# Optimization experiments

Measured on AMD Instinct MI355X. Metric: run time of the kernel, lower is better.

Reference implementation:

```python
import jax, jax.numpy as jnp
import numpy as np

E = 8        # num_sirens
F = 236      # siren_features (also per-expert output dim)
M = 441      # moe_features
C = 3        # input_size (coords)
OUT = 3      # output_size
HL = 3       # layersiren - 2 hidden sine layers
W0 = 30.0
N = 65536


def setup_inputs() -> dict:
    key = jax.random.key(0)
    ks = jax.random.split(key, 20)
    u = lambda k, shape, lim: jax.random.uniform(k, shape, jnp.float32, -lim, lim)
    sl = lambda fan_in: float(np.sqrt(6.0 / fan_in) / 30.0)  # sine_init limit
    inp = {}
    inp["x"] = jax.random.uniform(ks[0], (N, C), jnp.float32, -1.0, 1.0)
    # SIREN experts, stacked over E. First layer: first_layer_sine_init (1/fan_in).
    inp["siren_W1"] = u(ks[1], (E, C, F), 1.0 / C)
    inp["siren_b1"] = u(ks[2], (E, F), 1.0 / C)
    inp["siren_Wh"] = u(ks[3], (HL, E, F, F), sl(F))
    inp["siren_bh"] = u(ks[4], (HL, E, F), sl(F))
    inp["siren_Wo"] = u(ks[5], (E, F, F), sl(F))
    inp["siren_bo"] = u(ks[6], (E, F), sl(F))
    # Gating MLP (Moe): Linear(3,M)+ReLU, Linear(M,M)+ReLU, Linear(M,E)+Top1+Softmax
    inp["moe_W1"] = u(ks[7], (C, M), sl(C))
    inp["moe_b1"] = u(ks[8], (M,), sl(C))
    inp["moe_W2"] = u(ks[9], (M, M), sl(M))
    inp["moe_b2"] = u(ks[10], (M,), sl(M))
    inp["moe_W3"] = u(ks[11], (M, E), sl(M))
    inp["moe_b3"] = u(ks[12], (E,), sl(M))
    # Decoder: Linear(E*F, F)+ReLU, Linear(F, OUT)
    inp["dec_W1"] = u(ks[13], (E * F, F), sl(E * F))
    inp["dec_b1"] = u(ks[14], (F,), sl(E * F))
    inp["dec_W2"] = u(ks[15], (F, OUT), sl(F))
    inp["dec_b2"] = u(ks[16], (OUT,), sl(F))
    return inp


def reference(x, siren_W1, siren_b1, siren_Wh, siren_bh, siren_Wo, siren_bo,
              moe_W1, moe_b1, moe_W2, moe_b2, moe_W3, moe_b3,
              dec_W1, dec_b1, dec_W2, dec_b2):
    n = x.shape[0]
    # --- parallel SIREN experts, batched over E ---
    h = jnp.sin(W0 * (jnp.einsum('nc,ecf->enf', x, siren_W1) + siren_b1[:, None, :]))
    for i in range(HL):  # fixed small layer loop
        h = jnp.sin(W0 * (jnp.einsum('enf,efg->eng', h, siren_Wh[i]) + siren_bh[i][:, None, :]))
    so = jnp.einsum('enf,efg->eng', h, siren_Wo) + siren_bo[:, None, :]       # (E,N,F)
    siren_cat = jnp.transpose(so, (1, 0, 2)).reshape(n, E * F)                # cat along -1, expert-major
    # --- gating MLP + Top-1 + softmax ---
    g = jax.nn.relu(x @ moe_W1 + moe_b1)
    g = jax.nn.relu(g @ moe_W2 + moe_b2)
    logits = g @ moe_W3 + moe_b3                                              # (N,E)
    _, top_idx = jax.lax.top_k(logits, 1)
    mask = jnp.zeros_like(logits).at[jnp.arange(n)[:, None], top_idx].set(1.0)
    masked = jnp.where(mask > 0, logits, -jnp.inf)
    weights = jax.nn.softmax(masked, axis=-1)                                 # one-hot at argmax
    # --- KL(uniform || weights), batchmean (stored as self.kl_loss in torch) ---
    logw = jnp.log(weights + 1e-10)
    unif = jnp.asarray(1.0 / E, logw.dtype)
    kl = jnp.sum(unif * (jnp.log(unif) - logw)) / n
    # --- repeat_interleave(F) * concat, then decoder ---
    w_full = jnp.broadcast_to(weights[:, :, None], (n, E, F)).reshape(n, E * F)
    dec_in = w_full * siren_cat
    out = jax.nn.relu(dec_in @ dec_W1 + dec_b1) @ dec_W2 + dec_b2             # (N,OUT)
    return out, kl
```

## Files before the change

kernel.cpp:

```cpp
#include <hip/hip_runtime.h>
#include <cstdint>

typedef unsigned short ushort_t;
typedef short bf16x8 __attribute__((ext_vector_type(8)));
typedef unsigned short u16x8 __attribute__((ext_vector_type(8)));
typedef float f32x4 __attribute__((ext_vector_type(4)));

#define NPTS 65536
#define WS_CNT 0
#define WS_BKT 64
#define OFF_W2S 1048640
#define OFF_W3T 1450048
#define OFF_SWT 1464640
#define OFF_D2F 6379840
#define WS_FAST 6388032u
#define WS_SLOW (64 + 8 * NPTS * 2)

__device__ __forceinline__ float bf2f(ushort_t u) {
  union { unsigned u; float f; } c; c.u = ((unsigned)u) << 16; return c.f;
}
__device__ __forceinline__ ushort_t f2bf(float f) {
  union { float f; unsigned u; } c; c.f = f;
  unsigned u = c.u + 0x7fffu + ((c.u >> 16) & 1u);
  return (ushort_t)(u >> 16);
}
__device__ __forceinline__ float rbf(float v) { return bf2f(f2bf(v)); }
__device__ __forceinline__ bool nan_bits(float v) {
  union { float f; unsigned u; } c; c.f = v;
  return ((c.u >> 23) & 0xFFu) == 0xFFu && (c.u & 0x7FFFFFu) != 0u;
}

__global__ void k_sentinel(float* out) {
  if (threadIdx.x == 0) out[0] = 1.0e30f;
}


__global__ __launch_bounds__(256) void k_prep_fast(
    const float* __restrict__ sWh, const float* __restrict__ sWo,
    const float* __restrict__ dW1, const float* __restrict__ mW2,
    const float* __restrict__ mW3, const float* __restrict__ dW2,
    int* __restrict__ counts, ushort_t* __restrict__ W2S,
    ushort_t* __restrict__ w3T, ushort_t* __restrict__ swt,
    ushort_t* __restrict__ d2f, float* __restrict__ out)
{
  long gid = (long)blockIdx.x * 256 + threadIdx.x;
  long gs = (long)gridDim.x * 256;
  for (long i = gid; i < 40L * 61440; i += gs) {
    int mat = (int)(i / 61440);
    int f = (int)(i - (long)mat * 61440);
    int u = f & 7, ln = (f >> 3) & 63, kt = (f >> 9) & 7, t = f >> 12;
    int n = t * 16 + (ln & 15);
    int k = kt * 32 + (ln >> 4) * 8 + u;
    if (n >= 236 || k >= 236) swt[i] = 0;
  }
  for (long i = gid; i < 40L * 55696; i += gs) {
    int mat = (int)(i / 55696);
    int r = (int)(i - (long)mat * 55696);
    int k = r / 236, n = r - k * 236;
    const float* W = (mat < 24) ? (sWh + (long)mat * 55696)
                   : (mat < 32) ? (sWo + (long)(mat - 24) * 55696)
                                : (dW1 + (long)(mat - 32) * 55696);
    ushort_t v = f2bf(W[r]);
    int t = n >> 4, l15 = n & 15;
    int kt = k >> 5, rr = k & 31;
    long dst = (long)mat * 61440 + (t << 12) + (kt << 9) + ((((rr >> 3) << 4) + l15) << 3) + (rr & 7);
    swt[dst] = v;
  }
  for (long i = gid; i < 4096; i += gs) {
    int u = (int)(i & 7), lane = (int)((i >> 3) & 63), kt = (int)(i >> 9);
    int n = lane & 15, k = kt * 32 + ((lane >> 4) << 3) + u;
    d2f[i] = (n < 3 && k < 236) ? f2bf(dW2[k * 3 + n]) : (ushort_t)0;
  }
  for (long i = gid; i < 25088; i += gs) {
    int kt = (int)(i / (28 * 64));
    int rem = (int)(i - (long)kt * 28 * 64);
    int nt = rem / 64, lane = rem - nt * 64;
    int l15 = lane & 15, quad = lane >> 4;
    int n = nt * 16 + l15;
    u16x8 tv;
    #pragma unroll
    for (int u = 0; u < 8; ++u) {
      int k = kt * 32 + quad * 8 + u;
      tv[u] = (k < 441 && n < 441) ? f2bf(mW2[(long)k * 441 + n]) : (ushort_t)0;
    }
    *(u16x8*)(W2S + i * 8) = tv;
  }
  for (long i = gid; i < 7296; i += gs) {
    int e = (int)(i / 456), c = (int)(i - (long)e * 456);
    w3T[i] = (e < 8 && c < 441) ? f2bf(mW3[(long)c * 8 + e]) : (ushort_t)0;
  }
  if (gid < 8) counts[gid] = 0;
  if (gid == 8) out[NPTS * 3] = 18.125f;
}

__global__ __launch_bounds__(256) void k_gate_fast(
    const float* __restrict__ x,
    const float* __restrict__ mW1, const float* __restrict__ mb1,
    const float* __restrict__ mb2, const float* __restrict__ mb3,
    const ushort_t* __restrict__ W2S, const ushort_t* __restrict__ w3Tg,
    int* __restrict__ counts, ushort_t* __restrict__ bucket)
{
  __shared__ ushort_t At[64][40];
  __shared__ float W1c[1792];
  __shared__ float xl[192];
  __shared__ ushort_t chunkC[64][72];
  __shared__ ushort_t w3T[16][456];
  __shared__ float b2c[448];
  __shared__ unsigned char bexp[64];

  int tid = threadIdx.x;
  int blk = blockIdx.x;
  if (tid < 192) {
    int p = tid / 3, c = tid - p * 3;
    xl[tid] = rbf(x[(blk * 64 + p) * 3 + c]);
  }
  for (int j = tid; j < 1792; j += 256) {
    int c = j / 448, m = j - c * 448;
    float v = 0.f;
    if (m < 441) v = (c < 3) ? rbf(mW1[c * 441 + m]) : rbf(mb1[m]);
    W1c[j] = v;
  }
  for (int j = tid; j < 448; j += 256) b2c[j] = (j < 441) ? rbf(mb2[j]) : 0.f;
  for (int ch = tid; ch < 912; ch += 256)
    *(u16x8*)(&w3T[0][0] + ch * 8) = *(const u16x8*)(w3Tg + ch * 8);

  int w = tid >> 6, lane = tid & 63;
  int l15 = lane & 15, quad = lane >> 4;

  f32x4 acc[4][7];
  #pragma unroll
  for (int a = 0; a < 4; ++a)
    #pragma unroll
    for (int b = 0; b < 7; ++b)
      acc[a][b] = (f32x4){0.f, 0.f, 0.f, 0.f};

  int am = tid >> 2, ak = (tid & 3) * 8;

  for (int kt = 0; kt < 14; ++kt) {
    int kk0 = kt * 32;
    __syncthreads();
    {
      float x0 = xl[am * 3], x1 = xl[am * 3 + 1], x2 = xl[am * 3 + 2];
      u16x8 tmp;
      #pragma unroll
      for (int u = 0; u < 8; ++u) {
        int j = kk0 + ak + u;
        ushort_t h = 0;
        if (j < 441) {
          float t = x0 * W1c[j];
          t = fmaf(x1, W1c[448 + j], t);
          t = fmaf(x2, W1c[896 + j], t);
          t = rbf(t);
          t = rbf(t + W1c[1344 + j]);
          t = fmaxf(t, 0.f);
          h = f2bf(t);
        }
        tmp[u] = h;
      }
      *(u16x8*)(At[am] + ak) = tmp;
    }
    __syncthreads();
    bf16x8 bfr[7];
    #pragma unroll
    for (int j = 0; j < 7; ++j)
      bfr[j] = *(const bf16x8*)(W2S + ((kt * 28 + (w + 4 * j)) * 64 + lane) * 8);
    #pragma unroll
    for (int mt = 0; mt < 4; ++mt) {
      bf16x8 a = *(const bf16x8*)(&At[mt * 16 + l15][quad * 8]);
      #pragma unroll
      for (int j = 0; j < 7; ++j)
        acc[mt][j] = __builtin_amdgcn_mfma_f32_16x16x32_bf16(a, bfr[j], acc[mt][j], 0, 0, 0);
    }
  }

  f32x4 acc3[4];
  #pragma unroll
  for (int mt = 0; mt < 4; ++mt) acc3[mt] = (f32x4){0.f, 0.f, 0.f, 0.f};
  #pragma unroll
  for (int j = 0; j < 7; ++j) {
    __syncthreads();
    #pragma unroll
    for (int mt = 0; mt < 4; ++mt) {
      #pragma unroll
      for (int r = 0; r < 4; ++r) {
        int cg = j * 64 + w * 16 + l15;
        int m = mt * 16 + quad * 4 + r;
        float v = rbf(acc[mt][j][r]);
        v = rbf(v + b2c[cg]);
        v = fmaxf(v, 0.f);
        chunkC[m][w * 16 + l15] = f2bf(v);
      }
    }
    __syncthreads();
    bf16x8 b0 = *(const bf16x8*)(&w3T[l15][j * 64 + quad * 8]);
    bf16x8 b1 = *(const bf16x8*)(&w3T[l15][j * 64 + 32 + quad * 8]);
    #pragma unroll
    for (int mt = 0; mt < 4; ++mt) {
      bf16x8 a0 = *(const bf16x8*)(&chunkC[mt * 16 + l15][quad * 8]);
      bf16x8 a1 = *(const bf16x8*)(&chunkC[mt * 16 + l15][32 + quad * 8]);
      acc3[mt] = __builtin_amdgcn_mfma_f32_16x16x32_bf16(a0, b0, acc3[mt], 0, 0, 0);
      acc3[mt] = __builtin_amdgcn_mfma_f32_16x16x32_bf16(a1, b1, acc3[mt], 0, 0, 0);
    }
  }
  float b3v = (l15 < 8) ? rbf(mb3[l15]) : 0.f;
  if (w == 0) {
    #pragma unroll
    for (int mt = 0; mt < 4; ++mt) {
      #pragma unroll
      for (int r = 0; r < 4; ++r) {
        float lv = rbf(acc3[mt][r]);
        lv = rbf(lv + b3v);
        float v = (l15 < 8) ? lv : -1.0e30f;
        int ii = l15;
        #pragma unroll
        for (int mk = 1; mk < 8; mk <<= 1) {
          float ov = __shfl_xor(v, mk);
          int oi = __shfl_xor(ii, mk);
          if (ov > v || (ov == v && oi < ii)) { v = ov; ii = oi; }
        }
        if (l15 == 0) bexp[mt * 16 + quad * 4 + r] = (unsigned char)ii;
      }
    }
  }
  __syncthreads();
  if (tid < 64) {
    int bi = (int)bexp[tid];
    int slot = 0;
    #pragma unroll
    for (int ee = 0; ee < 8; ++ee) {
      unsigned long long msk = __ballot(bi == ee);
      if (bi == ee) {
        int leader = (int)__builtin_ctzll(msk);
        int rank = __popcll(msk & ((1ull << tid) - 1ull));
        int basep = 0;
        if (tid == leader) basep = atomicAdd(&counts[ee], __popcll(msk));
        basep = __shfl(basep, leader);
        slot = basep + rank;
      }
    }
    bucket[bi * NPTS + slot] = (ushort_t)(blk * 64 + tid);
  }
}

__global__ __launch_bounds__(256) void k_sdec_fast(
    const float* __restrict__ x,
    const float* __restrict__ sW1, const float* __restrict__ sb1,
    const float* __restrict__ sbh, const float* __restrict__ sbo,
    const float* __restrict__ db1, const float* __restrict__ db2,
    const ushort_t* __restrict__ swt, const ushort_t* __restrict__ d2f,
    const int* __restrict__ counts, const ushort_t* __restrict__ bucket,
    float* __restrict__ out)
{
  __shared__ ushort_t hA[64][264];
  __shared__ int idxl[64];
  __shared__ float xl[64][3];
  __shared__ float wc[944];

  int e = blockIdx.y;
  int base = blockIdx.x * 64;
  int cnt = counts[e];
  if (base >= cnt) return;
  int np = min(64, cnt - base);
  int tid = threadIdx.x;

  if (tid < 64) {
    int s = base + (tid < np ? tid : 0);
    idxl[tid] = (int)bucket[e * NPTS + s];
  }
  __syncthreads();
  if (tid < 192) {
    int p = tid / 3, c = tid - p * 3;
    xl[p][c] = rbf(x[idxl[p] * 3 + c]);
  }
  for (int j = tid; j < 944; j += 256)
    wc[j] = (j < 708) ? rbf(sW1[e * 708 + j]) : 30.f * rbf(sb1[e * 236 + (j - 708)]);
  __syncthreads();

  int w = tid >> 6, lane = tid & 63;
  int l15 = lane & 15, quad = lane >> 4;

  for (int i = lane; i < 16 * 264; i += 64) {
    int pr = i / 264, f = i - pr * 264;
    int p = w * 16 + pr;
    ushort_t hv = 0;
    if (f < 236) {
      float v = xl[p][0] * wc[f];
      v = fmaf(xl[p][1], wc[236 + f], v);
      v = fmaf(xl[p][2], wc[472 + f], v);
      v = fmaf(30.f, v, wc[708 + f]);
      hv = f2bf(__sinf(v));
    }
    hA[p][f] = hv;
  }
  __syncthreads();

  for (int l = 0; l < 5; ++l) {
    const ushort_t* Wt; const float* bias; int act;
    if (l < 3)       { Wt = swt + (l * 8 + e) * 61440; bias = sbh + (l * 8 + e) * 236; act = 0; }
    else if (l == 3) { Wt = swt + (24 + e) * 61440;    bias = sbo + e * 236;           act = 1; }
    else             { Wt = swt + (32 + e) * 61440;    bias = db1;                     act = 2; }

    bf16x8 afr[4][8];
    #pragma unroll
    for (int mt = 0; mt < 4; ++mt)
      #pragma unroll
      for (int kt = 0; kt < 8; ++kt)
        afr[mt][kt] = *(const bf16x8*)(&hA[mt * 16 + l15][kt * 32 + quad * 8]);
    __syncthreads();

    #pragma unroll
    for (int tt = 0; tt < 4; ++tt) {
      int t = w + tt * 4;
      if (t < 15) {
        f32x4 acc[4];
        #pragma unroll
        for (int mt = 0; mt < 4; ++mt) acc[mt] = (f32x4){0.f, 0.f, 0.f, 0.f};
        #pragma unroll
        for (int kt = 0; kt < 8; ++kt) {
          bf16x8 b = *(const bf16x8*)(Wt + ((t * 8 + kt) * 64 + lane) * 8);
          #pragma unroll
          for (int mt = 0; mt < 4; ++mt)
            acc[mt] = __builtin_amdgcn_mfma_f32_16x16x32_bf16(afr[mt][kt], b, acc[mt], 0, 0, 0);
        }
        int n = t * 16 + l15;
        if (n < 236) {
          float bv = rbf(bias[n]);
          float b30 = 30.f * bv;
          #pragma unroll
          for (int mt = 0; mt < 4; ++mt) {
            #pragma unroll
            for (int r = 0; r < 4; ++r) {
              int m = mt * 16 + quad * 4 + r;
              float v;
              if (act == 0)      v = __sinf(fmaf(30.f, acc[mt][r], b30));
              else if (act == 1) v = acc[mt][r] + bv;
              else               v = fmaxf(acc[mt][r] + bv, 0.f);
              hA[m][n] = f2bf(v);
            }
          }
        }
      }
    }
    __syncthreads();
  }

  {
    f32x4 acc = (f32x4){0.f, 0.f, 0.f, 0.f};
    #pragma unroll
    for (int kt = 0; kt < 8; ++kt) {
      bf16x8 a = *(const bf16x8*)(&hA[w * 16 + l15][kt * 32 + quad * 8]);
      bf16x8 b = *(const bf16x8*)(d2f + (kt * 64 + lane) * 8);
      acc = __builtin_amdgcn_mfma_f32_16x16x32_bf16(a, b, acc, 0, 0, 0);
    }
    if (l15 < 3) {
      float bv = rbf(db2[l15]);
      #pragma unroll
      for (int r = 0; r < 4; ++r) {
        int p = w * 16 + quad * 4 + r;
        if (p < np) {
          float s = acc[r] + bv;
          out[idxl[p] * 3 + l15] = nan_bits(s) ? 16.0f : fminf(fmaxf(s, -4.f), 4.f);
        }
      }
    }
  }
}


__global__ void k_prep_slow(int* counts, float* out) {
  int t = threadIdx.x;
  if (t < 8) counts[t] = 0;
  if (t == 8) out[NPTS * 3] = 18.125f;
}

__global__ __launch_bounds__(256) void k_gate_slow(
    const float* __restrict__ x,
    const float* __restrict__ mW1, const float* __restrict__ mb1,
    const float* __restrict__ mW2, const float* __restrict__ mb2,
    const float* __restrict__ mW3, const float* __restrict__ mb3,
    int* __restrict__ counts, ushort_t* __restrict__ bucket)
{
  extern __shared__ char smem[];
  ushort_t* At  = (ushort_t*)smem;
  ushort_t* Bt  = (ushort_t*)(smem + 5120);
  float*    W1c = (float*)(smem + 40960);
  ushort_t* g2  = (ushort_t*)smem;
  float*    b2c = (float*)(smem + 58368);
  float*    xl  = (float*)(smem + 60160);
  float*    lg  = (float*)(smem + 60928);

  int tid = threadIdx.x;
  int blk = blockIdx.x;
  if (tid < 192) {
    int p = tid / 3, c = tid - p * 3;
    xl[tid] = rbf(x[(blk * 64 + p) * 3 + c]);
  }
  for (int j = tid; j < 1792; j += 256) {
    int c = j / 448, m = j - c * 448;
    float v = 0.f;
    if (m < 441) v = (c < 3) ? rbf(mW1[c * 441 + m]) : rbf(mb1[m]);
    W1c[j] = v;
  }
  for (int j = tid; j < 448; j += 256) b2c[j] = (j < 441) ? rbf(mb2[j]) : 0.f;

  int w = tid >> 6, lane = tid & 63;
  int l15 = lane & 15, quad = lane >> 4;

  f32x4 acc[4][7];
  #pragma unroll
  for (int a = 0; a < 4; ++a)
    #pragma unroll
    for (int b = 0; b < 7; ++b)
      acc[a][b] = (f32x4){0.f, 0.f, 0.f, 0.f};

  int am = tid >> 2, ak = (tid & 3) * 8;

  for (int kt = 0; kt < 14; ++kt) {
    int kk0 = kt * 32;
    __syncthreads();
    {
      float x0 = xl[am * 3], x1 = xl[am * 3 + 1], x2 = xl[am * 3 + 2];
      u16x8 tmp;
      #pragma unroll
      for (int u = 0; u < 8; ++u) {
        int j = kk0 + ak + u;
        ushort_t h = 0;
        if (j < 441) {
          float t = x0 * W1c[j];
          t = fmaf(x1, W1c[448 + j], t);
          t = fmaf(x2, W1c[896 + j], t);
          t = rbf(t);
          t = rbf(t + W1c[1344 + j]);
          t = fmaxf(t, 0.f);
          h = f2bf(t);
        }
        tmp[u] = h;
      }
      *(u16x8*)(At + am * 40 + ak) = tmp;
    }
    {
      int n1 = tid;
      #pragma unroll
      for (int q = 0; q < 4; ++q) {
        u16x8 tv;
        #pragma unroll
        for (int u = 0; u < 8; ++u) {
          int kk = kk0 + q * 8 + u;
          tv[u] = (kk < 441 && n1 < 441) ? f2bf(mW2[kk * 441 + n1]) : (ushort_t)0;
        }
        *(u16x8*)(Bt + n1 * 40 + q * 8) = tv;
      }
      int n2 = tid + 256;
      if (n2 < 448) {
        #pragma unroll
        for (int q = 0; q < 4; ++q) {
          u16x8 tv;
          #pragma unroll
          for (int u = 0; u < 8; ++u) {
            int kk = kk0 + q * 8 + u;
            tv[u] = (kk < 441 && n2 < 441) ? f2bf(mW2[kk * 441 + n2]) : (ushort_t)0;
          }
          *(u16x8*)(Bt + n2 * 40 + q * 8) = tv;
        }
      }
    }
    __syncthreads();
    bf16x8 bfr[7];
    #pragma unroll
    for (int j = 0; j < 7; ++j) {
      int nt = w + 4 * j;
      bfr[j] = *(const bf16x8*)(Bt + (nt * 16 + l15) * 40 + quad * 8);
    }
    #pragma unroll
    for (int mt = 0; mt < 4; ++mt) {
      bf16x8 a = *(const bf16x8*)(At + (mt * 16 + l15) * 40 + quad * 8);
      #pragma unroll
      for (int j = 0; j < 7; ++j)
        acc[mt][j] = __builtin_amdgcn_mfma_f32_16x16x32_bf16(a, bfr[j], acc[mt][j], 0, 0, 0);
    }
  }
  __syncthreads();
  #pragma unroll
  for (int mt = 0; mt < 4; ++mt) {
    #pragma unroll
    for (int j = 0; j < 7; ++j) {
      int c = (w + 4 * j) * 16 + l15;
      float bv = b2c[c];
      #pragma unroll
      for (int r = 0; r < 4; ++r) {
        int m = mt * 16 + quad * 4 + r;
        float v = rbf(acc[mt][j][r]);
        v = rbf(v + bv);
        v = fmaxf(v, 0.f);
        g2[m * 456 + c] = f2bf(v);
      }
    }
  }
  __syncthreads();
  {
    int m3 = tid >> 2, eg = tid & 3;
    float s0 = 0.f, s1 = 0.f;
    const ushort_t* row = g2 + m3 * 456;
    for (int j = 0; j < 441; ++j) {
      float gv = bf2f(row[j]);
      s0 = fmaf(gv, rbf(mW3[j * 8 + 2 * eg]), s0);
      s1 = fmaf(gv, rbf(mW3[j * 8 + 2 * eg + 1]), s1);
    }
    s0 = rbf(rbf(s0) + rbf(mb3[2 * eg]));
    s1 = rbf(rbf(s1) + rbf(mb3[2 * eg + 1]));
    lg[m3 * 8 + 2 * eg] = s0;
    lg[m3 * 8 + 2 * eg + 1] = s1;
  }
  __syncthreads();
  if (tid < 64) {
    float best = lg[tid * 8];
    int bi = 0;
    #pragma unroll
    for (int e = 1; e < 8; ++e) {
      float v = lg[tid * 8 + e];
      if (v > best) { best = v; bi = e; }
    }
    int slot = 0;
    #pragma unroll
    for (int e = 0; e < 8; ++e) {
      unsigned long long msk = __ballot(bi == e);
      if (bi == e) {
        int leader = (int)__builtin_ctzll(msk);
        int rank = __popcll(msk & ((1ull << tid) - 1ull));
        int basep = 0;
        if (tid == leader) basep = atomicAdd(&counts[e], __popcll(msk));
        basep = __shfl(basep, leader);
        slot = basep + rank;
      }
    }
    bucket[bi * NPTS + slot] = (ushort_t)(blk * 64 + tid);
  }
}

__global__ __launch_bounds__(256) void k_sdec_slow(
    const float* __restrict__ x,
    const float* __restrict__ sW1, const float* __restrict__ sb1,
    const float* __restrict__ sWh, const float* __restrict__ sbh,
    const float* __restrict__ sWo, const float* __restrict__ sbo,
    const float* __restrict__ dW1, const float* __restrict__ db1,
    const float* __restrict__ dW2, const float* __restrict__ db2,
    const int* __restrict__ counts, const ushort_t* __restrict__ bucket,
    float* __restrict__ out)
{
  __shared__ ushort_t hA[64][264];
  __shared__ ushort_t wb[2][16][264];
  __shared__ int idxl[64];
  __shared__ float xl[64][3];
  __shared__ float wc[944];

  int e = blockIdx.y;
  int base = blockIdx.x * 64;
  int cnt = counts[e];
  if (base >= cnt) return;
  int np = min(64, cnt - base);
  int tid = threadIdx.x;

  if (tid < 64) {
    int s = base + (tid < np ? tid : 0);
    idxl[tid] = (int)bucket[e * NPTS + s];
  }
  __syncthreads();
  if (tid < 192) {
    int p = tid / 3, c = tid - p * 3;
    xl[p][c] = rbf(x[idxl[p] * 3 + c]);
  }
  for (int j = tid; j < 944; j += 256)
    wc[j] = (j < 708) ? rbf(sW1[e * 708 + j]) : rbf(sb1[e * 236 + (j - 708)]);
  for (int t = tid; t < 64 * 28; t += 256) {
    int p = t / 28, cc = 236 + (t - p * 28);
    hA[p][cc] = 0;
  }
  __syncthreads();
  for (int t = tid; t < 64 * 236; t += 256) {
    int p = t / 236, f = t - p * 236;
    float v = xl[p][0] * wc[f];
    v = fmaf(xl[p][1], wc[236 + f], v);
    v = fmaf(xl[p][2], wc[472 + f], v);
    v = rbf(v);
    v = rbf(v + wc[708 + f]);
    v = rbf(30.f * v);
    hA[p][f] = f2bf(sinf(v));
  }

  int w = tid >> 6, lane = tid & 63;
  int l15 = lane & 15, quad = lane >> 4;

  auto stage = [&](const float* W, int t, ushort_t (*buf)[264]) {
    int k = tid;
    if (k < 236) {
      const float* srcW = W + k * 236 + t * 16;
      int jmax = 236 - t * 16; if (jmax > 16) jmax = 16;
      float tv[16];
      if (jmax == 16) {
        *(f32x4*)(tv)      = *(const f32x4*)(srcW);
        *(f32x4*)(tv + 4)  = *(const f32x4*)(srcW + 4);
        *(f32x4*)(tv + 8)  = *(const f32x4*)(srcW + 8);
        *(f32x4*)(tv + 12) = *(const f32x4*)(srcW + 12);
      } else {
        *(f32x4*)(tv)      = *(const f32x4*)(srcW);
        *(f32x4*)(tv + 4)  = *(const f32x4*)(srcW + 4);
        *(f32x4*)(tv + 8)  = *(const f32x4*)(srcW + 8);
        tv[12] = tv[13] = tv[14] = tv[15] = 0.f;
      }
      #pragma unroll
      for (int j = 0; j < 16; ++j)
        buf[j][k] = (j < jmax) ? f2bf(tv[j]) : (ushort_t)0;
    } else {
      #pragma unroll
      for (int j = 0; j < 16; ++j) buf[j][k] = 0;
    }
  };

  for (int l = 0; l < 5; ++l) {
    const float* W; const float* bias; int act;
    if (l < 3)       { W = sWh + (l * 8 + e) * 55696; bias = sbh + (l * 8 + e) * 236; act = 0; }
    else if (l == 3) { W = sWo + e * 55696;           bias = sbo + e * 236;           act = 1; }
    else             { W = dW1 + e * 55696;           bias = db1;                     act = 2; }

    __syncthreads();
    bf16x8 afr[4][8];
    #pragma unroll
    for (int mt = 0; mt < 4; ++mt)
      #pragma unroll
      for (int kt = 0; kt < 8; ++kt)
        afr[mt][kt] = *(const bf16x8*)(&hA[mt * 16 + l15][kt * 32 + quad * 8]);
    stage(W, 0, wb[0]);
    __syncthreads();

    for (int t = 0; t < 15; ++t) {
      if (t < 14) stage(W, t + 1, wb[(t + 1) & 1]);
      if ((t & 3) == w) {
        f32x4 acc[4];
        #pragma unroll
        for (int mt = 0; mt < 4; ++mt) acc[mt] = (f32x4){0.f, 0.f, 0.f, 0.f};
        #pragma unroll
        for (int kt = 0; kt < 8; ++kt) {
          bf16x8 b = *(const bf16x8*)(&wb[t & 1][l15][kt * 32 + quad * 8]);
          #pragma unroll
          for (int mt = 0; mt < 4; ++mt)
            acc[mt] = __builtin_amdgcn_mfma_f32_16x16x32_bf16(afr[mt][kt], b, acc[mt], 0, 0, 0);
        }
        int n = t * 16 + l15;
        if (n < 236) {
          float bv = rbf(bias[n]);
          #pragma unroll
          for (int mt = 0; mt < 4; ++mt) {
            #pragma unroll
            for (int r = 0; r < 4; ++r) {
              int m = mt * 16 + quad * 4 + r;
              float v = rbf(acc[mt][r]);
              v = rbf(v + bv);
              if (act == 0) { v = rbf(30.f * v); v = sinf(v); }
              else if (act == 2) v = fmaxf(v, 0.f);
              hA[m][n] = f2bf(v);
            }
          }
        }
      }
      __syncthreads();
    }
  }

  for (int j = tid; j < 711; j += 256)
    wc[j] = (j < 708) ? rbf(dW2[j]) : rbf(db2[j - 708]);
  __syncthreads();
  if (tid < 192) {
    int p = tid / 3, o = tid - p * 3;
    if (p < np) {
      float s = 0.f;
      for (int k = 0; k < 236; ++k)
        s = fmaf(bf2f(hA[p][k]), wc[k * 3 + o], s);
      s = rbf(s);
      s = rbf(s + wc[708 + o]);
      out[idxl[p] * 3 + o] = nan_bits(s) ? 16.0f : fminf(fmaxf(s, -4.f), 4.f);
    }
  }
}

extern "C" void kernel_launch(void* const* d_in, const int* in_sizes, int n_in,
                              void* d_out, int out_size, void* d_ws, size_t ws_size,
                              hipStream_t stream) {
  const float* x   = (const float*)d_in[0];
  const float* sW1 = (const float*)d_in[1];
  const float* sb1 = (const float*)d_in[2];
  const float* sWh = (const float*)d_in[3];
  const float* sbh = (const float*)d_in[4];
  const float* sWo = (const float*)d_in[5];
  const float* sbo = (const float*)d_in[6];
  const float* mW1 = (const float*)d_in[7];
  const float* mb1 = (const float*)d_in[8];
  const float* mW2 = (const float*)d_in[9];
  const float* mb2 = (const float*)d_in[10];
  const float* mW3 = (const float*)d_in[11];
  const float* mb3 = (const float*)d_in[12];
  const float* dW1 = (const float*)d_in[13];
  const float* db1 = (const float*)d_in[14];
  const float* dW2 = (const float*)d_in[15];
  const float* db2 = (const float*)d_in[16];

  float* outp = (float*)d_out;
  char* ws = (char*)d_ws;
  int* counts      = (int*)(ws + WS_CNT);
  ushort_t* bucket = (ushort_t*)(ws + WS_BKT);

  if (ws_size >= (size_t)WS_FAST) {
    ushort_t* W2S = (ushort_t*)(ws + OFF_W2S);
    ushort_t* w3T = (ushort_t*)(ws + OFF_W3T);
    ushort_t* swt = (ushort_t*)(ws + OFF_SWT);
    ushort_t* d2f = (ushort_t*)(ws + OFF_D2F);
    k_prep_fast<<<dim3(2048), dim3(256), 0, stream>>>(sWh, sWo, dW1, mW2, mW3, dW2,
                                                      counts, W2S, w3T, swt, d2f, outp);
    k_gate_fast<<<dim3(1024), dim3(256), 0, stream>>>(x, mW1, mb1, mb2, mb3,
                                                      W2S, w3T, counts, bucket);
    k_sdec_fast<<<dim3(1024, 8), dim3(256), 0, stream>>>(x, sW1, sb1, sbh, sbo,
                                                         db1, db2, swt, d2f,
                                                         counts, bucket, outp);
  } else if (ws_size >= (size_t)WS_SLOW) {
    k_prep_slow<<<dim3(1), dim3(64), 0, stream>>>(counts, outp);
    k_gate_slow<<<dim3(1024), dim3(256), 62976, stream>>>(x, mW1, mb1, mW2, mb2, mW3, mb3,
                                                          counts, bucket);
    k_sdec_slow<<<dim3(1024, 8), dim3(256), 0, stream>>>(x, sW1, sb1, sWh, sbh, sWo, sbo,
                                                         dW1, db1, dW2, db2, counts, bucket, outp);
  } else {
    k_sentinel<<<dim3(1), dim3(64), 0, stream>>>(outp);
  }
}
```

Baseline: 284.7 us.

## Compact expert-block grid and vectorize weight swizzle in prep kernel

The siren/decoder kernel now launches a flat grid of 1032 blocks, and each block finds its expert and offset from a prefix scan over the per-expert counts. This replaces the 1024x8 grid, where most blocks exited early, and removes the cost of launching and scheduling about 8k mostly empty blocks. The weight prep loop is also rewritten so each thread gathers 8 bf16 values and writes one 16-byte vector, instead of a separate zero-fill pass followed by scattered 2-byte stores. In exchange, the reads from the source weights are strided, and the grid size assumes at most 1032 non-empty blocks in total.

```diff
diff --git a/kernel.cpp b/kernel.cpp
--- a/kernel.cpp
+++ b/kernel.cpp
@@ -45,26 +45,24 @@
 {
   long gid = (long)blockIdx.x * 256 + threadIdx.x;
   long gs = (long)gridDim.x * 256;
-  for (long i = gid; i < 40L * 61440; i += gs) {
-    int mat = (int)(i / 61440);
-    int f = (int)(i - (long)mat * 61440);
-    int u = f & 7, ln = (f >> 3) & 63, kt = (f >> 9) & 7, t = f >> 12;
-    int n = t * 16 + (ln & 15);
-    int k = kt * 32 + (ln >> 4) * 8 + u;
-    if (n >= 236 || k >= 236) swt[i] = 0;
-  }
-  for (long i = gid; i < 40L * 55696; i += gs) {
-    int mat = (int)(i / 55696);
-    int r = (int)(i - (long)mat * 55696);
-    int k = r / 236, n = r - k * 236;
+  for (long i = gid; i < 307200; i += gs) {
+    int mat = (int)(i / 7680);
+    int r = (int)(i - (long)mat * 7680);
+    int t = r >> 9;
+    int r2 = r & 511;
+    int kt = r2 >> 6, lane = r2 & 63;
+    int n = t * 16 + (lane & 15);
+    int q = lane >> 4;
     const float* W = (mat < 24) ? (sWh + (long)mat * 55696)
                    : (mat < 32) ? (sWo + (long)(mat - 24) * 55696)
                                 : (dW1 + (long)(mat - 32) * 55696);
-    ushort_t v = f2bf(W[r]);
-    int t = n >> 4, l15 = n & 15;
-    int kt = k >> 5, rr = k & 31;
-    long dst = (long)mat * 61440 + (t << 12) + (kt << 9) + ((((rr >> 3) << 4) + l15) << 3) + (rr & 7);
-    swt[dst] = v;
+    u16x8 tv;
+    #pragma unroll
+    for (int u = 0; u < 8; ++u) {
+      int k = kt * 32 + q * 8 + u;
+      tv[u] = (n < 236 && k < 236) ? f2bf(W[k * 236 + n]) : (ushort_t)0;
+    }
+    *(u16x8*)(swt + i * 8) = tv;
   }
   for (long i = gid; i < 4096; i += gs) {
     int u = (int)(i & 7), lane = (int)((i >> 3) & 63), kt = (int)(i >> 9);
@@ -256,11 +254,17 @@
   __shared__ float xl[64][3];
   __shared__ float wc[944];
 
-  int e = blockIdx.y;
-  int base = blockIdx.x * 64;
-  int cnt = counts[e];
-  if (base >= cnt) return;
-  int np = min(64, cnt - base);
+  int b = blockIdx.x;
+  int e = -1, base = 0, cnte = 0, cum = 0;
+  #pragma unroll
+  for (int ee = 0; ee < 8; ++ee) {
+    int c = counts[ee];
+    int nb = (c + 63) >> 6;
+    if (e < 0 && b < cum + nb) { e = ee; base = (b - cum) << 6; cnte = c; }
+    cum += nb;
+  }
+  if (e < 0) return;
+  int np = min(64, cnte - base);
   int tid = threadIdx.x;
 
   if (tid < 64) {
@@ -317,10 +321,10 @@
         for (int mt = 0; mt < 4; ++mt) acc[mt] = (f32x4){0.f, 0.f, 0.f, 0.f};
         #pragma unroll
         for (int kt = 0; kt < 8; ++kt) {
-          bf16x8 b = *(const bf16x8*)(Wt + ((t * 8 + kt) * 64 + lane) * 8);
+          bf16x8 bb = *(const bf16x8*)(Wt + ((t * 8 + kt) * 64 + lane) * 8);
           #pragma unroll
           for (int mt = 0; mt < 4; ++mt)
-            acc[mt] = __builtin_amdgcn_mfma_f32_16x16x32_bf16(afr[mt][kt], b, acc[mt], 0, 0, 0);
+            acc[mt] = __builtin_amdgcn_mfma_f32_16x16x32_bf16(afr[mt][kt], bb, acc[mt], 0, 0, 0);
         }
         int n = t * 16 + l15;
         if (n < 236) {
@@ -349,8 +353,8 @@
     #pragma unroll
     for (int kt = 0; kt < 8; ++kt) {
       bf16x8 a = *(const bf16x8*)(&hA[w * 16 + l15][kt * 32 + quad * 8]);
-      bf16x8 b = *(const bf16x8*)(d2f + (kt * 64 + lane) * 8);
-      acc = __builtin_amdgcn_mfma_f32_16x16x32_bf16(a, b, acc, 0, 0, 0);
+      bf16x8 bb = *(const bf16x8*)(d2f + (kt * 64 + lane) * 8);
+      acc = __builtin_amdgcn_mfma_f32_16x16x32_bf16(a, bb, acc, 0, 0, 0);
     }
     if (l15 < 3) {
       float bv = rbf(db2[l15]);
@@ -717,9 +721,9 @@
                                                       counts, W2S, w3T, swt, d2f, outp);
     k_gate_fast<<<dim3(1024), dim3(256), 0, stream>>>(x, mW1, mb1, mb2, mb3,
                                                       W2S, w3T, counts, bucket);
-    k_sdec_fast<<<dim3(1024, 8), dim3(256), 0, stream>>>(x, sW1, sb1, sbh, sbo,
-                                                         db1, db2, swt, d2f,
-                                                         counts, bucket, outp);
+    k_sdec_fast<<<dim3(1032), dim3(256), 0, stream>>>(x, sW1, sb1, sbh, sbo,
+                                                      db1, db2, swt, d2f,
+                                                      counts, bucket, outp);
   } else if (ws_size >= (size_t)WS_SLOW) {
     k_prep_slow<<<dim3(1), dim3(64), 0, stream>>>(counts, outp);
     k_gate_slow<<<dim3(1024), dim3(256), 62976, stream>>>(x, mW1, mb1, mW2, mb2, mW3, mb3,
```

Result: no change. 281.7 us (median of 3 runs) (-1.1%).
